# Kernel optimization log

Hardware: AMD Instinct MI355X
Metric: run time of the kernel (lower is better)

The kernel has to match this reference:

```python
import jax, jax.numpy as jnp
import numpy as np

N_NODES = 50000
N_EDGES = 1600000
F_IN, F_HID, F_MID = 264, 48, 64


def setup_inputs() -> dict:
    key = jax.random.key(0)
    ks = jax.random.split(key, 12)
    def lin(kw, fan_in, fan_out):
        s = 1.0 / np.sqrt(fan_in)
        return jax.random.uniform(kw, (fan_in, fan_out), jnp.float32, -s, s)
    return {
        "x": jax.random.normal(ks[0], (N_NODES, F_IN), jnp.float32),
        "edge_index": jax.random.randint(ks[1], (2, N_EDGES), 0, N_NODES, jnp.int64),
        "edge_weight": jax.random.uniform(ks[2], (N_EDGES,), jnp.float32, 0.01, 1.0),
        "WM": lin(ks[3], F_IN, F_HID), "bM": jnp.zeros((F_HID,), jnp.float32),
        "WA": lin(ks[4], F_IN, F_HID), "bA": jnp.zeros((F_HID,), jnp.float32),
        "WS": lin(ks[5], F_IN, F_HID), "bS": jnp.zeros((F_HID,), jnp.float32),
        "W1": lin(ks[6], 3 * F_HID, F_MID), "b1": jnp.zeros((F_MID,), jnp.float32),
        "W2": lin(ks[7], F_MID, 1), "b2": jnp.zeros((1,), jnp.float32),
    }


def _gcn_norm(edge_index, edge_weight, n):
    # add self-loops with weight 1 (PyG gcn_norm default)
    loop = jnp.arange(n, dtype=edge_index.dtype)
    row = jnp.concatenate([edge_index[0], loop])
    col = jnp.concatenate([edge_index[1], loop])
    w = jnp.concatenate([edge_weight, jnp.ones((n,), edge_weight.dtype)])
    deg = jax.ops.segment_sum(w, col, num_segments=n)
    dis = jnp.where(deg > 0, jax.lax.rsqrt(jnp.where(deg > 0, deg, 1.0)), 0.0)
    norm = dis[row] * w * dis[col]
    return row, col, norm


def reference(x, edge_index, edge_weight, WM, bM, WA, bA, WS, bS, W1, b1, W2, b2):
    n = x.shape[0]
    row, col, norm = _gcn_norm(edge_index, edge_weight, n)

    # GCNConv aggr='max': linear (no bias) -> gather -> weighted scatter-max -> +bias
    hM = x @ WM                              # [N, 48]
    msgM = norm[:, None] * hM[row]           # [E+N, 48]
    outM = jax.ops.segment_max(msgM, col, num_segments=n) + bM
    xConvM = jax.nn.relu(outM)

    # GCNConv aggr='add'
    hA = x @ WA
    msgA = norm[:, None] * hA[row]
    outA = jax.ops.segment_sum(msgA, col, num_segments=n) + bA
    xConvA = jax.nn.relu(outA)

    # plain linear branch
    xLin = jax.nn.relu(x @ WS + bS)

    h = jnp.concatenate([xConvM, xConvA, xLin], axis=1)  # [N, 144]
    h = jax.nn.relu(h @ W1 + b1)
    out = h @ W2 + b2                         # [N, 1]
    return out.squeeze(-1)
```

## Files before the change

### kernel.cpp

```cpp
#include <hip/hip_runtime.h>
#include <stdint.h>

#define N_NODES 50000
#define N_EDGES 1600000
#define F_IN    264
#define F_HID   48
#define F_CAT   144
#define F_MID   64
#define K_PAD   288
#define K_MLP   160

#define BSH     6
#define NB      782
#define NBP     1024
#define CHUNK   2048
#define NCHUNK  ((N_EDGES + CHUNK - 1) / CHUNK)
#define SCAN_BLOCKS ((NB * 64 + 255) / 256)

typedef unsigned short u16;
typedef unsigned int   u32;

using short8  = __attribute__((ext_vector_type(8))) short;
using floatx4 = __attribute__((ext_vector_type(4))) float;
using floatx2 = __attribute__((ext_vector_type(2))) float;
using uintx4  = __attribute__((ext_vector_type(4))) u32;

__device__ __forceinline__ float bf2f(u16 u) {
    return __uint_as_float(((u32)u) << 16);
}
__device__ __forceinline__ u16 f2bf(float f) {
    u32 u = __float_as_uint(f);
    u32 r = (u + 0x7fffu + ((u >> 16) & 1u)) >> 16;
    return (u16)r;
}
__device__ __forceinline__ float ldf(const void* p, size_t i, int isbf) {
    return isbf ? bf2f(((const u16*)p)[i]) : ((const float*)p)[i];
}
__device__ __forceinline__ uintx4 s8_to_u4(short8 v) {
    union { short8 s; uintx4 u; } c; c.s = v; return c.u;
}

__device__ __forceinline__ int ld_row(const int* ei, int e, int is64) {
    return is64 ? ei[2 * (size_t)e] : ei[e];
}
__device__ __forceinline__ int ld_col(const int* ei, int e, int is64) {
    return is64 ? ei[2 * ((size_t)N_EDGES + e)] : ei[(size_t)N_EDGES + e];
}

__global__ __launch_bounds__(256)
void k_prep(const void* __restrict__ WM, const void* __restrict__ WA,
            const void* __restrict__ WS, const void* __restrict__ W1,
            const void* __restrict__ bM, const void* __restrict__ bA,
            const void* __restrict__ b1, const void* __restrict__ W2,
            const void* __restrict__ b2,
            u16* __restrict__ Wt, u16* __restrict__ W1bt,
            float* __restrict__ bMf, float* __restrict__ bAf,
            float* __restrict__ b1f, float* __restrict__ W2f,
            float* __restrict__ b2f,
            const u16* __restrict__ xu, const int* __restrict__ ei,
            int* __restrict__ flags, u32* __restrict__ cnt) {
    __shared__ int sfl[2];
    const int tid = threadIdx.x;
    if (tid < 64) {
        u16 h = xu[2 * tid];
        u32 E = (h >> 7) & 0xFF;
        int sane = (h == 0) || (E >= 90 && E <= 140);
        unsigned long long m = __ballot(sane);
        int z = (tid < 16) ? ei[2 * tid + 1] : 0;
        unsigned long long nz = __ballot(z != 0);
        if (tid == 0) {
            sfl[0] = (__popcll(m) >= 48) ? 1 : 0;
            sfl[1] = (nz == 0ull) ? 1 : 0;
        }
    }
    __syncthreads();
    const int isbf = sfl[0];
    if (blockIdx.x == 0 && tid == 0) {
        flags[0] = sfl[0]; flags[1] = sfl[1]; cnt[0] = 0u;
    }
    int t = blockIdx.x * 256 + tid;
    if (t < F_CAT * K_PAD) {
        int n = t / K_PAD, k = t - n * K_PAD;
        u16 v = 0;
        if (k < F_IN) {
            const void* W = (n < 48) ? WM : (n < 96) ? WA : WS;
            int nn = (n < 48) ? n : (n < 96) ? n - 48 : n - 96;
            if (isbf) v = ((const u16*)W)[(size_t)k * 48 + nn];
            else      v = f2bf(((const float*)W)[(size_t)k * 48 + nn]);
        }
        Wt[(size_t)n * K_PAD + k] = v;
        return;
    }
    t -= F_CAT * K_PAD;
    if (t < F_MID * K_MLP) {
        int j = t / K_MLP, k = t - j * K_MLP;
        u16 v = 0;
        if (k < F_CAT) {
            if (isbf) v = ((const u16*)W1)[(size_t)k * F_MID + j];
            else      v = f2bf(((const float*)W1)[(size_t)k * F_MID + j]);
        }
        W1bt[t] = v;
        return;
    }
    t -= F_MID * K_MLP;
    if (t < 48)            { bMf[t] = ldf(bM, t, isbf); return; }
    t -= 48;
    if (t < 48)            { bAf[t] = ldf(bA, t, isbf); return; }
    t -= 48;
    if (t < 64)            { b1f[t] = ldf(b1, t, isbf); return; }
    t -= 64;
    if (t < 64)            { W2f[t] = ldf(W2, t, isbf); return; }
    t -= 64;
    if (t < 1)             { b2f[0] = ldf(b2, 0, isbf); return; }
}

__global__ __launch_bounds__(256)
void k_bhist(const int* __restrict__ ei, u32* __restrict__ bhist,
             const int* __restrict__ flags) {
    const int is64 = flags[1];
    __shared__ u32 hist[NB];
    for (int j = threadIdx.x; j < NB; j += 256) hist[j] = 0;
    __syncthreads();
    int e0 = blockIdx.x * CHUNK;
    for (int i = 0; i < CHUNK / 256; ++i) {
        int e = e0 + i * 256 + threadIdx.x;
        if (e < N_EDGES) {
            int c = ld_col(ei, e, is64);
            atomicAdd(&hist[(u32)c >> BSH], 1u);
        }
    }
    __syncthreads();
    for (int j = threadIdx.x; j < NB; j += 256)
        bhist[(size_t)j * NCHUNK + blockIdx.x] = hist[j];
}

__global__ __launch_bounds__(256)
void k_bscan(u32* __restrict__ bhist, u32* __restrict__ bsum,
             u32* __restrict__ boff, u32* __restrict__ cnt) {
    const int tid  = threadIdx.x;
    const int wid  = (blockIdx.x * 256 + tid) >> 6;
    const int lane = tid & 63;
    __shared__ int lastFlag;
    __shared__ u32 wsum2[4];
    if (wid < NB) {
        u32* row = bhist + (size_t)wid * NCHUNK;
        u32 run = 0;
        for (int i0 = 0; i0 < NCHUNK; i0 += 64) {
            int i = i0 + lane;
            u32 v = (i < NCHUNK) ? row[i] : 0u;
            u32 sc = v;
#pragma unroll
            for (int off = 1; off < 64; off <<= 1) {
                u32 t2 = (u32)__shfl_up((int)sc, off, 64);
                if (lane >= off) sc += t2;
            }
            if (i < NCHUNK) row[i] = run + sc - v;
            run += (u32)__shfl((int)sc, 63, 64);
        }
        if (lane == 0)
            __hip_atomic_store(&bsum[wid], run, __ATOMIC_RELAXED,
                               __HIP_MEMORY_SCOPE_AGENT);
    }
    __syncthreads();
    if (tid == 0) {
        __threadfence();
        u32 old = __hip_atomic_fetch_add(cnt, 1u, __ATOMIC_ACQ_REL,
                                         __HIP_MEMORY_SCOPE_AGENT);
        lastFlag = (old == (u32)(SCAN_BLOCKS - 1));
    }
    __syncthreads();
    if (!lastFlag) return;
    u32 a[4];
#pragma unroll
    for (int u = 0; u < 4; ++u) {
        int i = 4 * tid + u;
        a[u] = (i < NB) ? __hip_atomic_load(&bsum[i], __ATOMIC_RELAXED,
                                            __HIP_MEMORY_SCOPE_AGENT) : 0u;
    }
    u32 s = a[0] + a[1] + a[2] + a[3];
    u32 sc = s;
#pragma unroll
    for (int off = 1; off < 64; off <<= 1) {
        u32 t2 = (u32)__shfl_up((int)sc, off, 64);
        if ((tid & 63) >= off) sc += t2;
    }
    if ((tid & 63) == 63) wsum2[tid >> 6] = sc;
    __syncthreads();
    u32 wbase = 0;
    for (int wv = 0; wv < (tid >> 6); ++wv) wbase += wsum2[wv];
    u32 excl = wbase + sc - s;
    int i0 = 4 * tid;
    u32 b0 = excl, b1 = excl + a[0], b2 = excl + a[0] + a[1],
        b3 = excl + a[0] + a[1] + a[2];
    if (i0     <= NB) boff[i0]     = b0;
    if (i0 + 1 <= NB) boff[i0 + 1] = b1;
    if (i0 + 2 <= NB) boff[i0 + 2] = b2;
    if (i0 + 3 <= NB) boff[i0 + 3] = b3;
}

__global__ __launch_bounds__(256)
void k_bplace(const int* __restrict__ ei, const void* __restrict__ ew,
              const u32* __restrict__ bhist, const u32* __restrict__ boff,
              int2* __restrict__ bpair, const int* __restrict__ flags) {
    const int isbf = flags[0], is64 = flags[1];
    const int blk = blockIdx.x;
    const int tid = threadIdx.x;
    __shared__ int2 stage[CHUNK];
    __shared__ u32 lcur[NBP];
    __shared__ u32 lbase[NBP];
    __shared__ u32 wsum[4];
    for (int j = tid; j < NBP; j += 256) lcur[j] = 0;
    __syncthreads();
    const int e0 = blk * CHUNK;
    u32 cv[CHUNK / 256];
#pragma unroll
    for (int i = 0; i < CHUNK / 256; ++i) {
        int e = e0 + i * 256 + tid;
        u32 c = 0xFFFFFFFFu;
        if (e < N_EDGES) {
            c = (u32)ld_col(ei, e, is64);
            atomicAdd(&lcur[c >> BSH], 1u);
        }
        cv[i] = c;
    }
    __syncthreads();
    {
        u32 a0 = lcur[4 * tid], a1 = lcur[4 * tid + 1];
        u32 a2 = lcur[4 * tid + 2], a3 = lcur[4 * tid + 3];
        u32 s = a0 + a1 + a2 + a3;
        u32 sc = s;
        int lane = tid & 63;
#pragma unroll
        for (int off = 1; off < 64; off <<= 1) {
            u32 t = (u32)__shfl_up((int)sc, off, 64);
            if (lane >= off) sc += t;
        }
        if (lane == 63) wsum[tid >> 6] = sc;
        __syncthreads();
        u32 wbase = 0;
        for (int wv = 0; wv < (tid >> 6); ++wv) wbase += wsum[wv];
        u32 excl = wbase + sc - s;
        lbase[4 * tid]     = excl;
        lbase[4 * tid + 1] = excl + a0;
        lbase[4 * tid + 2] = excl + a0 + a1;
        lbase[4 * tid + 3] = excl + a0 + a1 + a2;
        __syncthreads();
        lcur[4 * tid]     = excl;
        lcur[4 * tid + 1] = excl + a0;
        lcur[4 * tid + 2] = excl + a0 + a1;
        lcur[4 * tid + 3] = excl + a0 + a1 + a2;
    }
    __syncthreads();
#pragma unroll
    for (int i = 0; i < CHUNK / 256; ++i) {
        if (cv[i] != 0xFFFFFFFFu) {
            int e = e0 + i * 256 + tid;
            u32 c = cv[i];
            u32 j = c >> BSH;
            int r = ld_row(ei, e, is64);
            float w = ldf(ew, e, isbf);
            u32 slot = atomicAdd(&lcur[j], 1u);
            stage[slot] = make_int2(r | (int)((c & 63u) << 16) | (int)(j << 22),
                                    __float_as_int(w));
        }
    }
    __syncthreads();
    int tot = N_EDGES - e0; if (tot > CHUNK) tot = CHUNK;
    for (int i = tid; i < tot; i += 256) {
        int2 e2 = stage[i];
        u32 j = (u32)e2.x >> 22;
        u32 tgt = boff[j] + bhist[(size_t)j * NCHUNK + blk] + ((u32)i - lbase[j]);
        bpair[tgt] = e2;
    }
}

__global__ __launch_bounds__(256)
void k_bcsr(const int2* __restrict__ bpair, const u32* __restrict__ boff,
            int* __restrict__ rowptr, int2* __restrict__ csr_pair,
            float* __restrict__ dis) {
    const int b   = blockIdx.x;
    const int tid = threadIdx.x;
    const u32 base = boff[b];
    const u32 n    = boff[b + 1] - base;
    const int c0   = b << BSH;
    __shared__ u32 chist[64], pcur[64], pbeg[64];
    if (tid < 64) chist[tid] = 0;
    __syncthreads();
    for (u32 i = tid; i < n; i += 256)
        atomicAdd(&chist[((u32)bpair[base + i].x >> 16) & 63u], 1u);
    __syncthreads();
    if (tid < 64) {
        u32 v = chist[tid];
        u32 sc = v;
        for (int off = 1; off < 64; off <<= 1) {
            u32 t = (u32)__shfl_up((int)sc, off, 64);
            if (tid >= off) sc += t;
        }
        u32 excl = sc - v;
        pcur[tid] = excl;
        pbeg[tid] = excl;
        int c = c0 + tid;
        if (c <= N_NODES) rowptr[c] = (int)(base + excl);
    }
    __syncthreads();
    for (u32 i = tid; i < n; i += 256) {
        int2 e2 = bpair[base + i];
        u32 lc = ((u32)e2.x >> 16) & 63u;
        u32 lr = atomicAdd(&pcur[lc], 1u);
        csr_pair[base + lr] = make_int2(e2.x & 0xFFFF, e2.y);
    }
    __syncthreads();
    int j = tid >> 2, sub = tid & 3;
    int c = c0 + j;
    if (c < N_NODES) {
        u32 s0 = base + pbeg[j], s1 = base + pcur[j];
        float s = 0.f;
        for (u32 i = s0 + sub; i < s1; i += 4)
            s += __int_as_float(csr_pair[i].y);
        s += __shfl_down(s, 2, 4);
        s += __shfl_down(s, 1, 4);
        if (sub == 0) dis[c] = rsqrtf(1.0f + s);
    }
}

__global__ __launch_bounds__(256)
void k_gemm(const void* __restrict__ x, const u16* __restrict__ Wt,
            u16* __restrict__ hMB, u16* __restrict__ hFull,
            const void* __restrict__ bS, const int* __restrict__ flags) {
    const int isbf = flags[0];
    const int lane = threadIdx.x & 63;
    const int wave = threadIdx.x >> 6;
    const int mrow = lane & 15;
    const int q    = lane >> 4;
    const int m_base = blockIdx.x * 128 + wave * 32;

    floatx4 acc[2][9];
#pragma unroll
    for (int tt = 0; tt < 2; ++tt)
#pragma unroll
        for (int t = 0; t < 9; ++t) {
            acc[tt][t][0]=0.f; acc[tt][t][1]=0.f; acc[tt][t][2]=0.f; acc[tt][t][3]=0.f;
        }

    for (int k0 = 0; k0 < K_PAD; k0 += 32) {
        int k = k0 + q * 8;
        short8 a[2];
#pragma unroll
        for (int tt = 0; tt < 2; ++tt) {
            int node = m_base + tt * 16 + mrow;
            short8 av = {0,0,0,0,0,0,0,0};
            if (node < N_NODES && k < F_IN) {
                if (isbf) {
                    av = *(const short8*)((const u16*)x + (size_t)node * F_IN + k);
                } else {
                    const float* xf = (const float*)x + (size_t)node * F_IN + k;
                    floatx4 v0 = *(const floatx4*)xf;
                    floatx4 v1 = *(const floatx4*)(xf + 4);
                    av[0]=(short)f2bf(v0[0]); av[1]=(short)f2bf(v0[1]);
                    av[2]=(short)f2bf(v0[2]); av[3]=(short)f2bf(v0[3]);
                    av[4]=(short)f2bf(v1[0]); av[5]=(short)f2bf(v1[1]);
                    av[6]=(short)f2bf(v1[2]); av[7]=(short)f2bf(v1[3]);
                }
            }
            a[tt] = av;
        }
#pragma unroll
        for (int t = 0; t < 9; ++t) {
            short8 b = *(const short8*)(Wt + (size_t)(t * 16 + mrow) * K_PAD + k);
            acc[0][t] = __builtin_amdgcn_mfma_f32_16x16x32_bf16(a[0], b, acc[0][t], 0, 0, 0);
            acc[1][t] = __builtin_amdgcn_mfma_f32_16x16x32_bf16(a[1], b, acc[1][t], 0, 0, 0);
        }
    }
#pragma unroll
    for (int tt = 0; tt < 2; ++tt)
#pragma unroll
    for (int t = 0; t < 9; ++t) {
        int n = t * 16 + mrow;
#pragma unroll
        for (int r = 0; r < 4; ++r) {
            int row = m_base + tt * 16 + q * 4 + r;
            if (row < N_NODES) {
                float v = acc[tt][t][r];
                if (n < 96) hMB[(size_t)row * 96 + n] = f2bf(v);
                else        hFull[(size_t)row * F_CAT + n] =
                                f2bf(fmaxf(v + ldf(bS, n - 96, isbf), 0.f));
            }
        }
    }
}

__global__ __launch_bounds__(256)
void k_agg(const u16* __restrict__ hMB, u16* __restrict__ hFull,
           const int* __restrict__ rowptr, const int2* __restrict__ csr_pair,
           const float* __restrict__ dis,
           const float* __restrict__ bMf, const float* __restrict__ bAf) {
    const int lane = threadIdx.x & 63;
    const int wave = threadIdx.x >> 6;
    const int node = blockIdx.x * 4 + wave;

    const int g = lane / 12;
    const int s = lane - g * 12;
    const bool active = lane < 60;
    const bool isMax = s < 6;

    const int start = rowptr[node];
    const int end   = rowptr[node + 1];
    const float dn  = dis[node];
    const float dn2 = dn * dn;
    const float padnm = isMax ? dn2 : 0.f;

    const u32 s16     = 16u * (u32)s;
    const u32 selfOff = __umul24((u32)node, 192u) + s16;

    floatx2 acc2[4];
    {
        short8 rv0 = *(const short8*)((const char*)hMB + selfOff);
        uintx4 w4 = s8_to_u4(rv0);
        float seed = (isMax || g == 0) ? dn2 : 0.f;
#pragma unroll
        for (int p = 0; p < 4; ++p) {
            acc2[p][0] = seed * __uint_as_float(w4[p] << 16);
            acc2[p][1] = seed * __uint_as_float(w4[p] & 0xffff0000u);
        }
    }

    for (int c0 = start; c0 < end; c0 += 64) {
        int cl = end - c0; if (cl > 64) cl = 64;
        int li = lane < cl ? lane : cl - 1;
        int2 mp = csr_pair[c0 + li];
        float disr = dis[mp.x];
        float mynm = __int_as_float(mp.y) * disr * dn;
        u32 myoff  = __umul24((u32)mp.x, 192u);

        for (int j = 0; j < cl; j += 20) {
            u32 offv[4]; float nmv[4];
#pragma unroll
            for (int u = 0; u < 4; ++u) {
                int el = j + 5 * u + g;
                bool valid = active && (el < cl);
                int elc = (el < cl) ? el : 0;
                u32 off  = (u32)__shfl((int)myoff, elc, 64) + s16;
                float nm = __shfl(mynm, elc, 64);
                offv[u] = valid ? off : selfOff;
                nmv[u]  = valid ? nm  : padnm;
            }
            short8 rv[4];
#pragma unroll
            for (int u = 0; u < 4; ++u)
                rv[u] = *(const short8*)((const char*)hMB + offv[u]);
#pragma unroll
            for (int u = 0; u < 4; ++u) {
                uintx4 w4 = s8_to_u4(rv[u]);
                floatx2 nm2; nm2[0] = nmv[u]; nm2[1] = nmv[u];
#pragma unroll
                for (int p = 0; p < 4; ++p) {
                    floatx2 f;
                    f[0] = __uint_as_float(w4[p] << 16);
                    f[1] = __uint_as_float(w4[p] & 0xffff0000u);
                    if (isMax) {
                        floatx2 m = nm2 * f;
                        acc2[p][0] = fmaxf(acc2[p][0], m[0]);
                        acc2[p][1] = fmaxf(acc2[p][1], m[1]);
                    } else {
                        acc2[p] += nm2 * f;
                    }
                }
            }
        }
    }

#pragma unroll
    for (int gg = 1; gg < 5; ++gg) {
        int src = lane + 12 * gg;
        floatx2 t[4];
#pragma unroll
        for (int p = 0; p < 4; ++p) {
            t[p][0] = __shfl(acc2[p][0], src, 64);
            t[p][1] = __shfl(acc2[p][1], src, 64);
        }
        if (lane < 12) {
            if (isMax) {
#pragma unroll
                for (int p = 0; p < 4; ++p) {
                    acc2[p][0] = fmaxf(acc2[p][0], t[p][0]);
                    acc2[p][1] = fmaxf(acc2[p][1], t[p][1]);
                }
            } else {
#pragma unroll
                for (int p = 0; p < 4; ++p) acc2[p] += t[p];
            }
        }
    }

    if (lane < 12) {
        const float* bp = isMax ? (bMf + 8 * lane) : (bAf + 8 * lane - 48);
        short8 hv;
#pragma unroll
        for (int p = 0; p < 4; ++p) {
            hv[2 * p]     = (short)f2bf(fmaxf(acc2[p][0] + bp[2 * p],     0.f));
            hv[2 * p + 1] = (short)f2bf(fmaxf(acc2[p][1] + bp[2 * p + 1], 0.f));
        }
        *(short8*)(hFull + (size_t)node * F_CAT + 8 * lane) = hv;
    }
}

__global__ __launch_bounds__(256)
void k_mlp(const u16* __restrict__ hFull, const u16* __restrict__ W1bt,
           const float* __restrict__ b1f, const float* __restrict__ W2f,
           const float* __restrict__ b2f, void* __restrict__ out,
           const int* __restrict__ flags) {
    const int isbf = flags[0];
    const int lane = threadIdx.x & 63;
    const int wave = threadIdx.x >> 6;
    const int mrow = lane & 15;
    const int q    = lane >> 4;
    const int m_base = blockIdx.x * 64 + wave * 16;
    const int node = m_base + mrow;

    floatx4 acc[4];
#pragma unroll
    for (int t = 0; t < 4; ++t) { acc[t][0]=0.f; acc[t][1]=0.f; acc[t][2]=0.f; acc[t][3]=0.f; }

    for (int k0 = 0; k0 < K_MLP; k0 += 32) {
        int k = k0 + q * 8;
        short8 a = {0,0,0,0,0,0,0,0};
        if (node < N_NODES && k < F_CAT)
            a = *(const short8*)(hFull + (size_t)node * F_CAT + k);
#pragma unroll
        for (int t = 0; t < 4; ++t) {
            short8 b = *(const short8*)(W1bt + (size_t)(t * 16 + mrow) * K_MLP + k);
            acc[t] = __builtin_amdgcn_mfma_f32_16x16x32_bf16(a, b, acc[t], 0, 0, 0);
        }
    }

    float pr[4] = {0.f, 0.f, 0.f, 0.f};
#pragma unroll
    for (int t = 0; t < 4; ++t) {
        int n = t * 16 + mrow;
        float b1v = b1f[n], w2v = W2f[n];
#pragma unroll
        for (int r = 0; r < 4; ++r)
            pr[r] += fmaxf(acc[t][r] + b1v, 0.f) * w2v;
    }
#pragma unroll
    for (int mask = 1; mask < 16; mask <<= 1)
#pragma unroll
        for (int r = 0; r < 4; ++r) pr[r] += __shfl_xor(pr[r], mask, 64);
    if (mrow == 0) {
#pragma unroll
        for (int r = 0; r < 4; ++r) {
            int nd = m_base + q * 4 + r;
            if (nd < N_NODES) {
                float res = pr[r] + b2f[0];
                if (isbf) ((u16*)out)[nd] = f2bf(res);
                else      ((float*)out)[nd] = res;
            }
        }
    }
}

extern "C" void kernel_launch(void* const* d_in, const int* in_sizes, int n_in,
                              void* d_out, int out_size, void* d_ws, size_t ws_size,
                              hipStream_t stream) {
    const void* x  = d_in[0];
    const int*  ei = (const int*)d_in[1];
    const void* ew = d_in[2];
    const void* WM = d_in[3];
    const void* bM = d_in[4];
    const void* WA = d_in[5];
    const void* bA = d_in[6];
    const void* WS = d_in[7];
    const void* bS = d_in[8];
    const void* W1 = d_in[9];
    const void* b1 = d_in[10];
    const void* W2 = d_in[11];
    const void* b2 = d_in[12];

    char* p = (char*)d_ws;
    auto alloc = [&](size_t bytes) -> char* {
        char* r = p; p += (bytes + 255) & ~(size_t)255; return r;
    };
    int*   flags    = (int*)  alloc(16);
    u32*   cnt      = (u32*)  alloc(16);
    float* dis      = (float*)alloc((size_t)N_NODES * 4);
    int*   rowptr   = (int*)  alloc((size_t)(N_NODES + 1) * 4);
    int2*  csr_pair = (int2*) alloc((size_t)N_EDGES * 8);
    u16*   hMB      = (u16*)  alloc((size_t)N_NODES * 96 * 2);
    u16*   hFull    = (u16*)  alloc((size_t)N_NODES * F_CAT * 2);
    u16*   Wt       = (u16*)  alloc((size_t)F_CAT * K_PAD * 2);
    u16*   W1bt    = (u16*)  alloc((size_t)F_MID * K_MLP * 2);
    u32*   bhist    = (u32*)  alloc((size_t)NB * NCHUNK * 4);
    u32*   bsum     = (u32*)  alloc((size_t)NB * 4);
    u32*   boff     = (u32*)  alloc((size_t)(NB + 1) * 4);
    float* bMf      = (float*)alloc(48 * 4);
    float* bAf      = (float*)alloc(48 * 4);
    float* b1f      = (float*)alloc(64 * 4);
    float* W2f      = (float*)alloc(64 * 4);
    float* b2f      = (float*)alloc(4);
    int2*  bpair    = (int2*)hMB;

    k_prep  <<<(F_CAT * K_PAD + F_MID * K_MLP + 225 + 255) / 256, 256, 0, stream>>>(
                 WM, WA, WS, W1, bM, bA, b1, W2, b2,
                 Wt, W1bt, bMf, bAf, b1f, W2f, b2f,
                 (const u16*)x, ei, flags, cnt);
    k_bhist <<<NCHUNK, 256, 0, stream>>>(ei, bhist, flags);
    k_bscan <<<SCAN_BLOCKS, 256, 0, stream>>>(bhist, bsum, boff, cnt);
    k_bplace<<<NCHUNK, 256, 0, stream>>>(ei, ew, bhist, boff, bpair, flags);
    k_bcsr  <<<NB, 256, 0, stream>>>(bpair, boff, rowptr, csr_pair, dis);
    k_gemm  <<<(N_NODES + 127) / 128, 256, 0, stream>>>(x, Wt, hMB, hFull, bS, flags);
    k_agg   <<<N_NODES / 4, 256, 0, stream>>>(hMB, hFull, rowptr, csr_pair, dis, bMf, bAf);
    k_mlp   <<<(N_NODES + 63) / 64, 256, 0, stream>>>(hFull, W1bt, b1f, W2f, b2f, d_out, flags);
    (void)in_sizes; (void)n_in; (void)out_size; (void)ws_size;
}
```

Measured before the change: 265.3 us.

## Fuse MLP head into aggregation kernel and compute degree sums in CSR build

Removes the separate MLP kernel: each aggregation wave now stages its node's 144-wide concatenated features in shared memory in fp32. Each lane then computes one of the 64 hidden units with a scalar FMA loop over W1, followed by a wave reduction against W2. This saves writing the conv halves of hFull and rereading all of it, plus one launch, but swaps MFMA for per-lane scalar FMAs and a W1 reload per node. The degree sum moves into the CSR scatter loop as a shared-memory float atomic, which drops a second pass over csr_pair. The edge chunk size is also doubled.

```diff
diff --git a/kernel.cpp b/kernel.cpp
--- a/kernel.cpp
+++ b/kernel.cpp
@@ -8,12 +8,11 @@
 #define F_CAT   144
 #define F_MID   64
 #define K_PAD   288
-#define K_MLP   160
 
 #define BSH     6
 #define NB      782
 #define NBP     1024
-#define CHUNK   2048
+#define CHUNK   4096
 #define NCHUNK  ((N_EDGES + CHUNK - 1) / CHUNK)
 #define SCAN_BLOCKS ((NB * 64 + 255) / 256)
 
@@ -53,7 +52,7 @@
             const void* __restrict__ bM, const void* __restrict__ bA,
             const void* __restrict__ b1, const void* __restrict__ W2,
             const void* __restrict__ b2,
-            u16* __restrict__ Wt, u16* __restrict__ W1bt,
+            u16* __restrict__ Wt, u16* __restrict__ W1c,
             float* __restrict__ bMf, float* __restrict__ bAf,
             float* __restrict__ b1f, float* __restrict__ W2f,
             float* __restrict__ b2f,
@@ -92,17 +91,12 @@
         return;
     }
     t -= F_CAT * K_PAD;
-    if (t < F_MID * K_MLP) {
-        int j = t / K_MLP, k = t - j * K_MLP;
-        u16 v = 0;
-        if (k < F_CAT) {
-            if (isbf) v = ((const u16*)W1)[(size_t)k * F_MID + j];
-            else      v = f2bf(((const float*)W1)[(size_t)k * F_MID + j]);
-        }
-        W1bt[t] = v;
+    if (t < F_CAT * F_MID) {
+        u16 v = isbf ? ((const u16*)W1)[t] : f2bf(((const float*)W1)[t]);
+        W1c[t] = v;
         return;
     }
-    t -= F_MID * K_MLP;
+    t -= F_CAT * F_MID;
     if (t < 48)            { bMf[t] = ldf(bM, t, isbf); return; }
     t -= 48;
     if (t < 48)            { bAf[t] = ldf(bA, t, isbf); return; }
@@ -283,8 +277,9 @@
     const u32 base = boff[b];
     const u32 n    = boff[b + 1] - base;
     const int c0   = b << BSH;
-    __shared__ u32 chist[64], pcur[64], pbeg[64];
-    if (tid < 64) chist[tid] = 0;
+    __shared__ u32 chist[64], pcur[64];
+    __shared__ float dsum[64];
+    if (tid < 64) { chist[tid] = 0u; dsum[tid] = 0.f; }
     __syncthreads();
     for (u32 i = tid; i < n; i += 256)
         atomicAdd(&chist[((u32)bpair[base + i].x >> 16) & 63u], 1u);
@@ -298,7 +293,6 @@
         }
         u32 excl = sc - v;
         pcur[tid] = excl;
-        pbeg[tid] = excl;
         int c = c0 + tid;
         if (c <= N_NODES) rowptr[c] = (int)(base + excl);
     }
@@ -308,18 +302,12 @@
         u32 lc = ((u32)e2.x >> 16) & 63u;
         u32 lr = atomicAdd(&pcur[lc], 1u);
         csr_pair[base + lr] = make_int2(e2.x & 0xFFFF, e2.y);
-    }
-    __syncthreads();
-    int j = tid >> 2, sub = tid & 3;
-    int c = c0 + j;
-    if (c < N_NODES) {
-        u32 s0 = base + pbeg[j], s1 = base + pcur[j];
-        float s = 0.f;
-        for (u32 i = s0 + sub; i < s1; i += 4)
-            s += __int_as_float(csr_pair[i].y);
-        s += __shfl_down(s, 2, 4);
-        s += __shfl_down(s, 1, 4);
-        if (sub == 0) dis[c] = rsqrtf(1.0f + s);
+        atomicAdd(&dsum[lc], __int_as_float(e2.y));
+    }
+    __syncthreads();
+    if (tid < 64) {
+        int c = c0 + tid;
+        if (c < N_NODES) dis[c] = rsqrtf(1.0f + dsum[tid]);
     }
 }
 
@@ -390,10 +378,13 @@
 }
 
 __global__ __launch_bounds__(256)
-void k_agg(const u16* __restrict__ hMB, u16* __restrict__ hFull,
+void k_agg(const u16* __restrict__ hMB, const u16* __restrict__ hFull,
            const int* __restrict__ rowptr, const int2* __restrict__ csr_pair,
            const float* __restrict__ dis,
-           const float* __restrict__ bMf, const float* __restrict__ bAf) {
+           const float* __restrict__ bMf, const float* __restrict__ bAf,
+           const u16* __restrict__ W1c, const float* __restrict__ b1f,
+           const float* __restrict__ W2f, const float* __restrict__ b2f,
+           void* __restrict__ out, const int* __restrict__ flags) {
     const int lane = threadIdx.x & 63;
     const int wave = threadIdx.x >> 6;
     const int node = blockIdx.x * 4 + wave;
@@ -411,6 +402,8 @@
 
     const u32 s16     = 16u * (u32)s;
     const u32 selfOff = __umul24((u32)node, 192u) + s16;
+
+    __shared__ float hsh[4][F_CAT];
 
     floatx2 acc2[4];
     {
@@ -494,68 +487,30 @@
 
     if (lane < 12) {
         const float* bp = isMax ? (bMf + 8 * lane) : (bAf + 8 * lane - 48);
-        short8 hv;
 #pragma unroll
         for (int p = 0; p < 4; ++p) {
-            hv[2 * p]     = (short)f2bf(fmaxf(acc2[p][0] + bp[2 * p],     0.f));
-            hv[2 * p + 1] = (short)f2bf(fmaxf(acc2[p][1] + bp[2 * p + 1], 0.f));
-        }
-        *(short8*)(hFull + (size_t)node * F_CAT + 8 * lane) = hv;
-    }
-}
-
-__global__ __launch_bounds__(256)
-void k_mlp(const u16* __restrict__ hFull, const u16* __restrict__ W1bt,
-           const float* __restrict__ b1f, const float* __restrict__ W2f,
-           const float* __restrict__ b2f, void* __restrict__ out,
-           const int* __restrict__ flags) {
-    const int isbf = flags[0];
-    const int lane = threadIdx.x & 63;
-    const int wave = threadIdx.x >> 6;
-    const int mrow = lane & 15;
-    const int q    = lane >> 4;
-    const int m_base = blockIdx.x * 64 + wave * 16;
-    const int node = m_base + mrow;
-
-    floatx4 acc[4];
-#pragma unroll
-    for (int t = 0; t < 4; ++t) { acc[t][0]=0.f; acc[t][1]=0.f; acc[t][2]=0.f; acc[t][3]=0.f; }
-
-    for (int k0 = 0; k0 < K_MLP; k0 += 32) {
-        int k = k0 + q * 8;
-        short8 a = {0,0,0,0,0,0,0,0};
-        if (node < N_NODES && k < F_CAT)
-            a = *(const short8*)(hFull + (size_t)node * F_CAT + k);
-#pragma unroll
-        for (int t = 0; t < 4; ++t) {
-            short8 b = *(const short8*)(W1bt + (size_t)(t * 16 + mrow) * K_MLP + k);
-            acc[t] = __builtin_amdgcn_mfma_f32_16x16x32_bf16(a, b, acc[t], 0, 0, 0);
-        }
-    }
-
-    float pr[4] = {0.f, 0.f, 0.f, 0.f};
-#pragma unroll
-    for (int t = 0; t < 4; ++t) {
-        int n = t * 16 + mrow;
-        float b1v = b1f[n], w2v = W2f[n];
-#pragma unroll
-        for (int r = 0; r < 4; ++r)
-            pr[r] += fmaxf(acc[t][r] + b1v, 0.f) * w2v;
-    }
-#pragma unroll
-    for (int mask = 1; mask < 16; mask <<= 1)
-#pragma unroll
-        for (int r = 0; r < 4; ++r) pr[r] += __shfl_xor(pr[r], mask, 64);
-    if (mrow == 0) {
-#pragma unroll
-        for (int r = 0; r < 4; ++r) {
-            int nd = m_base + q * 4 + r;
-            if (nd < N_NODES) {
-                float res = pr[r] + b2f[0];
-                if (isbf) ((u16*)out)[nd] = f2bf(res);
-                else      ((float*)out)[nd] = res;
-            }
-        }
+            hsh[wave][8 * lane + 2 * p]     = fmaxf(acc2[p][0] + bp[2 * p],     0.f);
+            hsh[wave][8 * lane + 2 * p + 1] = fmaxf(acc2[p][1] + bp[2 * p + 1], 0.f);
+        }
+    } else if (lane < 18) {
+        short8 hv = *(const short8*)(hFull + (size_t)node * F_CAT + 96 + 8 * (lane - 12));
+#pragma unroll
+        for (int j = 0; j < 8; ++j)
+            hsh[wave][96 + 8 * (lane - 12) + j] = bf2f((u16)hv[j]);
+    }
+    __syncthreads();
+
+    float mid = b1f[lane];
+#pragma unroll 8
+    for (int k = 0; k < F_CAT; ++k)
+        mid = __builtin_fmaf(hsh[wave][k], bf2f(W1c[(size_t)k * 64 + lane]), mid);
+    float val = fmaxf(mid, 0.f) * W2f[lane];
+#pragma unroll
+    for (int off = 32; off > 0; off >>= 1) val += __shfl_down(val, off, 64);
+    if (lane == 0) {
+        float res = val + b2f[0];
+        if (flags[0]) ((u16*)out)[node] = f2bf(res);
+        else          ((float*)out)[node] = res;
     }
 }
 
@@ -588,7 +543,7 @@
     u16*   hMB      = (u16*)  alloc((size_t)N_NODES * 96 * 2);
     u16*   hFull    = (u16*)  alloc((size_t)N_NODES * F_CAT * 2);
     u16*   Wt       = (u16*)  alloc((size_t)F_CAT * K_PAD * 2);
-    u16*   W1bt    = (u16*)  alloc((size_t)F_MID * K_MLP * 2);
+    u16*   W1c      = (u16*)  alloc((size_t)F_CAT * F_MID * 2);
     u32*   bhist    = (u32*)  alloc((size_t)NB * NCHUNK * 4);
     u32*   bsum     = (u32*)  alloc((size_t)NB * 4);
     u32*   boff     = (u32*)  alloc((size_t)(NB + 1) * 4);
@@ -599,16 +554,16 @@
     float* b2f      = (float*)alloc(4);
     int2*  bpair    = (int2*)hMB;
 
-    k_prep  <<<(F_CAT * K_PAD + F_MID * K_MLP + 225 + 255) / 256, 256, 0, stream>>>(
+    k_prep  <<<(F_CAT * K_PAD + F_CAT * F_MID + 225 + 255) / 256, 256, 0, stream>>>(
                  WM, WA, WS, W1, bM, bA, b1, W2, b2,
-                 Wt, W1bt, bMf, bAf, b1f, W2f, b2f,
+                 Wt, W1c, bMf, bAf, b1f, W2f, b2f,
                  (const u16*)x, ei, flags, cnt);
     k_bhist <<<NCHUNK, 256, 0, stream>>>(ei, bhist, flags);
     k_bscan <<<SCAN_BLOCKS, 256, 0, stream>>>(bhist, bsum, boff, cnt);
     k_bplace<<<NCHUNK, 256, 0, stream>>>(ei, ew, bhist, boff, bpair, flags);
     k_bcsr  <<<NB, 256, 0, stream>>>(bpair, boff, rowptr, csr_pair, dis);
     k_gemm  <<<(N_NODES + 127) / 128, 256, 0, stream>>>(x, Wt, hMB, hFull, bS, flags);
-    k_agg   <<<N_NODES / 4, 256, 0, stream>>>(hMB, hFull, rowptr, csr_pair, dis, bMf, bAf);
-    k_mlp   <<<(N_NODES + 63) / 64, 256, 0, stream>>>(hFull, W1bt, b1f, W2f, b2f, d_out, flags);
+    k_agg   <<<N_NODES / 4, 256, 0, stream>>>(hMB, hFull, rowptr, csr_pair, dis,
+                 bMf, bAf, W1c, b1f, W2f, b2f, d_out, flags);
     (void)in_sizes; (void)n_in; (void)out_size; (void)ws_size;
 }
```

Measured after the change: 297.3 us. +12.1%, slower.
